# Kernel optimization log

Measured on AMD Instinct MI355X. Metric: run time of the kernel, lower is better.

Reference implementation:

```python
import jax, jax.numpy as jnp
import numpy as np

B, N, K = 4, 2048, 32
CQ, CK, CV = 128, 128, 256
CQ1, CK1 = max(CQ, 32), max(CK, 32)
NUM_GROUPS = 32
EPS = 1e-5


def conv1x1(x, W, b):
    # x: [B,Cin,N,K], W: [Cout,Cin], b: [Cout]
    return jnp.einsum('oc,bcnk->bonk', W, x) + b[None, :, None, None]


def group_norm(x, gamma, beta, num_groups=NUM_GROUPS, eps=EPS):
    # x: [B,C,N,K]; stats over (C//G, N, K) per group, per sample (torch GroupNorm)
    b, c, n, k = x.shape
    xg = x.reshape(b, num_groups, c // num_groups, n, k)
    mean = xg.mean(axis=(2, 3, 4), keepdims=True)
    var = xg.var(axis=(2, 3, 4), keepdims=True)
    xg = (xg - mean) * jax.lax.rsqrt(var + eps)
    x = xg.reshape(b, c, n, k)
    return x * gamma[None, :, None, None] + beta[None, :, None, None]


def setup_inputs() -> dict:
    key = jax.random.key(0)
    ks = jax.random.split(key, 24)
    nrm = lambda k, shape, s=0.05: jax.random.normal(k, shape, jnp.float32) * s
    return {
        'feat': jax.random.normal(ks[0], (B, CQ, N), jnp.float32),
        'grouped_feat': jax.random.normal(ks[1], (B, CK, N, K), jnp.float32),
        'grouped_feat_out': jax.random.normal(ks[2], (B, CV, N, K), jnp.float32),
        'count': jax.random.randint(ks[3], (B, N), 0, K + 1, jnp.int32),
        'W_fc': nrm(ks[4], (CQ1, CQ)), 'b_fc': nrm(ks[5], (CQ1,)),
        'W_gc': nrm(ks[6], (CK1, CK)), 'b_gc': nrm(ks[7], (CK1,)),
        'g1': jnp.ones((CQ1 + CK1,), jnp.float32), 'be1': jnp.zeros((CQ1 + CK1,), jnp.float32),
        'W_w1': nrm(ks[8], (CV, CQ1 + CK1)), 'b_w1': nrm(ks[9], (CV,)),
        'g2': jnp.ones((CV,), jnp.float32), 'be2': jnp.zeros((CV,), jnp.float32),
        'W_w2': nrm(ks[10], (CV, CV)), 'b_w2': nrm(ks[11], (CV,)),
        'W_fo': nrm(ks[12], (CV, CV)), 'b_fo': nrm(ks[13], (CV,)),
        'g3': jnp.ones((CV,), jnp.float32), 'be3': jnp.zeros((CV,), jnp.float32),
    }


def reference(feat, grouped_feat, grouped_feat_out, count,
              W_fc, b_fc, W_gc, b_gc, g1, be1, W_w1, b_w1,
              g2, be2, W_w2, b_w2, W_fo, b_fo, g3, be3):
    # feat_conv (1x1 on [B,CQ,N,1]) then expand along K
    feat1 = jnp.einsum('oc,bcn->bon', W_fc, feat) + b_fc[None, :, None]  # [B,CQ1,N]
    feat1 = jnp.broadcast_to(feat1[..., None], (B, CQ1, N, K))
    gfeat1 = conv1x1(grouped_feat, W_gc, b_gc)  # [B,CK1,N,K]
    total = jnp.concatenate([feat1, gfeat1], axis=1)  # [B,CQ1+CK1,N,K]

    # weight_conv: ReLU -> GN -> Conv -> ReLU -> GN -> Conv
    x = jax.nn.relu(total)
    x = group_norm(x, g1, be1)
    x = conv1x1(x, W_w1, b_w1)
    x = jax.nn.relu(x)
    x = group_norm(x, g2, be2)
    scores = conv1x1(x, W_w2, b_w2)  # [B,CV,N,K]

    # count-based neighbor mask
    cnt = jnp.clip(count, 1, None)
    mask = (jnp.arange(K, dtype=cnt.dtype) < cnt[..., None]).astype(scores.dtype)  # [B,N,K]
    mask = mask[:, None]  # [B,1,N,K]
    scores = scores * mask + (-1e9) * (1.0 - mask)
    weight = jax.nn.softmax(scores, axis=-1)

    # feat_out_conv: Conv -> GN -> ReLU
    gout = conv1x1(grouped_feat_out, W_fo, b_fo)
    gout = jax.nn.relu(group_norm(gout, g3, be3))

    return (gout * weight).sum(axis=-1)  # [B,CV,N]
```

## Files before the change

kernel.cpp:

```cpp
#include <hip/hip_runtime.h>
#include <stdint.h>

#define DEVI __device__ __forceinline__

typedef __attribute__((ext_vector_type(4))) int    i32x4;
typedef __attribute__((ext_vector_type(4))) float  f32x4;
typedef __attribute__((ext_vector_type(8))) __bf16 bf16x8;

static constexpr int BB = 4, NN = 2048, KK = 32, PP = NN * KK;
static constexpr float GEPS = 1e-5f;

DEVI unsigned short f2bf(float f) {
  unsigned u = __builtin_bit_cast(unsigned, f);
  return (unsigned short)((u + 0x7FFFu + ((u >> 16) & 1u)) >> 16);
}
DEVI float bf2f(unsigned short h) {
  unsigned u = (unsigned)h << 16;
  return __builtin_bit_cast(float, u);
}
DEVI uint2 pack4(float a, float b, float c, float d) {
  return make_uint2((unsigned)f2bf(a) | ((unsigned)f2bf(b) << 16),
                    (unsigned)f2bf(c) | ((unsigned)f2bf(d) << 16));
}
DEVI void mfma16(f32x4& d, i32x4 a, i32x4 b) {
  d = __builtin_amdgcn_mfma_f32_16x16x32_bf16(
      __builtin_bit_cast(bf16x8, a), __builtin_bit_cast(bf16x8, b), d, 0, 0, 0);
}

__global__ void prep_kern(const float* Wfc, const float* Wgc, const float* Wfo,
                          unsigned short* dWfc, unsigned short* dWgc, unsigned short* dWfo) {
  int i = blockIdx.x * 256 + threadIdx.x;
  if (i < 16384)       dWfc[i] = f2bf(Wfc[i]);
  else if (i < 32768)  dWgc[i - 16384] = f2bf(Wgc[i - 16384]);
  else if (i < 98304)  dWfo[i - 32768] = f2bf(Wfo[i - 32768]);
}

template<int CIN, int COUT, int MODE, bool RELU>
__global__ __launch_bounds__(256, 2)
void gemm_kern(const void* srcA, const void* srcB,
               const unsigned short* Wmat, const float* bias,
               unsigned short* out, float* stats, int group_base,
               int P, int tiles_per_b, int nblk) {
  constexpr int MW = COUT / 4;
  constexpr int MF = MW / 16;
  constexpr int KS = CIN / 32;
  constexpr int CINP = CIN + 8;
  __shared__ unsigned short tile[64 * CINP];

  const int tid = threadIdx.x;
  const int lane = tid & 63, w = tid >> 6;
  const int l15 = lane & 15, lg = lane >> 4;
  const int b = blockIdx.x / nblk, blk = blockIdx.x % nblk;

  const unsigned short* Wb = (MODE == 1) ? (Wmat + (size_t)b * COUT * CIN) : Wmat;
  const float* biasb = (MODE == 1) ? (bias + b * COUT) : bias;

  i32x4 a[KS][MF];
#pragma unroll
  for (int ks = 0; ks < KS; ++ks)
#pragma unroll
    for (int mf = 0; mf < MF; ++mf)
      a[ks][mf] = *(const i32x4*)(Wb + (size_t)(w * MW + mf * 16 + l15) * CIN + ks * 32 + lg * 8);

  f32x4 bi[MF];
#pragma unroll
  for (int mf = 0; mf < MF; ++mf)
    bi[mf] = *(const f32x4*)(biasb + w * MW + mf * 16 + lg * 4);

  float ssum[MF], ssq[MF];
#pragma unroll
  for (int mf = 0; mf < MF; ++mf) { ssum[mf] = 0.f; ssq[mf] = 0.f; }

  for (int t = blk; t < tiles_per_b; t += nblk) {
    const int p0 = t * 64;
    if (MODE == 0) {
      const float* src = (const float*)srcA + (size_t)b * CIN * P + p0;
      const int cq = tid >> 4, pq = tid & 15;
#pragma unroll
      for (int cblk = 0; cblk < CIN; cblk += 64) {
        f32x4 v[4];
#pragma unroll
        for (int i = 0; i < 4; ++i)
          v[i] = *(const f32x4*)(src + (size_t)(cblk + cq * 4 + i) * (size_t)P + pq * 4);
#pragma unroll
        for (int jj = 0; jj < 4; ++jj) {
          uint2 pk = pack4(v[0][jj], v[1][jj], v[2][jj], v[3][jj]);
          *(uint2*)&tile[(pq * 4 + jj) * CINP + cblk + cq * 4] = pk;
        }
      }
    } else {
      const unsigned short* r1 = (const unsigned short*)srcA;
      const unsigned short* r2 = (const unsigned short*)srcB;
      const int cg = tid & 15, pq = tid >> 4;
#pragma unroll
      for (int cblk = 0; cblk < 256; cblk += 64) {
#pragma unroll
        for (int j = 0; j < 4; ++j) {
          int p = pq * 4 + j;
          const unsigned short* sp;
          if (cblk < 128) {
            int n = (p0 + p) >> 5;
            sp = r1 + ((size_t)b * NN + n) * 128 + cblk + cg * 4;
          } else {
            sp = r2 + ((size_t)b * PP + p0 + p) * 128 + (cblk - 128) + cg * 4;
          }
          *(uint2*)&tile[p * CINP + cblk + cg * 4] = *(const uint2*)sp;
        }
      }
    }
    __syncthreads();

    f32x4 acc[MF][4];
#pragma unroll
    for (int mf = 0; mf < MF; ++mf)
#pragma unroll
      for (int nf = 0; nf < 4; ++nf) acc[mf][nf] = f32x4{0.f, 0.f, 0.f, 0.f};

#pragma unroll
    for (int ks = 0; ks < KS; ++ks) {
      i32x4 bfr[4];
#pragma unroll
      for (int nf = 0; nf < 4; ++nf)
        bfr[nf] = *(const i32x4*)&tile[(nf * 16 + l15) * CINP + ks * 32 + lg * 8];
#pragma unroll
      for (int mf = 0; mf < MF; ++mf)
#pragma unroll
        for (int nf = 0; nf < 4; ++nf) mfma16(acc[mf][nf], a[ks][mf], bfr[nf]);
    }
    __syncthreads();

#pragma unroll
    for (int mf = 0; mf < MF; ++mf) {
      const int o4 = w * MW + mf * 16 + lg * 4;
#pragma unroll
      for (int nf = 0; nf < 4; ++nf) {
        const int p = p0 + nf * 16 + l15;
        float y0 = acc[mf][nf][0] + bi[mf][0];
        float y1 = acc[mf][nf][1] + bi[mf][1];
        float y2 = acc[mf][nf][2] + bi[mf][2];
        float y3 = acc[mf][nf][3] + bi[mf][3];
        if (RELU) {
          y0 = fmaxf(y0, 0.f); y1 = fmaxf(y1, 0.f);
          y2 = fmaxf(y2, 0.f); y3 = fmaxf(y3, 0.f);
        }
        ssum[mf] += y0 + y1 + y2 + y3;
        ssq[mf] += y0 * y0 + y1 * y1 + y2 * y2 + y3 * y3;
        *(uint2*)(out + ((size_t)b * P + p) * COUT + o4) = pack4(y0, y1, y2, y3);
      }
    }
  }

#pragma unroll
  for (int mf = 0; mf < MF; ++mf) {
    float s = ssum[mf], q = ssq[mf];
#pragma unroll
    for (int d = 1; d < 16; d <<= 1) { s += __shfl_xor(s, d); q += __shfl_xor(q, d); }
    if (l15 == 0) {
      int g = group_base + ((w * MW + mf * 16 + lg * 4) >> 3);
      atomicAdd(&stats[(b * 32 + g) * 2 + 0], s);
      atomicAdd(&stats[(b * 32 + g) * 2 + 1], q);
    }
  }
}

__global__ void fold1_kern(const float* st1, const float* g1, const float* be1,
                           const float* W_w1, const float* b_w1,
                           unsigned short* W1p, float* b1p) {
  int b = blockIdx.x, tid = threadIdx.x;
  __shared__ float s_l[256], t_l[256];
  {
    int c = tid, g = c >> 3;
    float cnt = (g < 16) ? (8.f * NN) : (8.f * NN * KK);
    float su = st1[(b * 32 + g) * 2], sq = st1[(b * 32 + g) * 2 + 1];
    float mean = su / cnt;
    float var = fmaxf(sq / cnt - mean * mean, 0.f);
    float s = g1[c] * rsqrtf(var + GEPS);
    s_l[c] = s; t_l[c] = be1[c] - mean * s;
  }
  __syncthreads();
  int o = tid;
  float acc = b_w1[o];
  for (int c = 0; c < 256; ++c) {
    float wv = W_w1[o * 256 + c];
    W1p[((size_t)b * 256 + o) * 256 + c] = f2bf(wv * s_l[c]);
    acc += wv * t_l[c];
  }
  b1p[b * 256 + o] = acc;
}

__global__ void fold23_kern(const float* st2, const float* st3,
                            const float* g2, const float* be2,
                            const float* W_w2, const float* b_w2,
                            const float* g3, const float* be3,
                            unsigned short* W2p, float* b2p, float* s3t3) {
  int b = blockIdx.x, tid = threadIdx.x;
  __shared__ float s_l[256], t_l[256];
  {
    int c = tid, g = c >> 3;
    float cnt = 8.f * NN * KK;
    float su = st2[(b * 32 + g) * 2], sq = st2[(b * 32 + g) * 2 + 1];
    float mean = su / cnt;
    float var = fmaxf(sq / cnt - mean * mean, 0.f);
    float s = g2[c] * rsqrtf(var + GEPS);
    s_l[c] = s; t_l[c] = be2[c] - mean * s;

    float su3 = st3[(b * 32 + g) * 2], sq3 = st3[(b * 32 + g) * 2 + 1];
    float mean3 = su3 / cnt;
    float var3 = fmaxf(sq3 / cnt - mean3 * mean3, 0.f);
    float s3 = g3[c] * rsqrtf(var3 + GEPS);
    s3t3[(b * 256 + c) * 2 + 0] = s3;
    s3t3[(b * 256 + c) * 2 + 1] = be3[c] - mean3 * s3;
  }
  __syncthreads();
  int o = tid;
  float acc = b_w2[o];
  for (int c = 0; c < 256; ++c) {
    float wv = W_w2[o * 256 + c];
    W2p[((size_t)b * 256 + o) * 256 + c] = f2bf(wv * s_l[c]);
    acc += wv * t_l[c];
  }
  b2p[b * 256 + o] = acc;
}

__global__ __launch_bounds__(256, 2)
void k5_kern(const unsigned short* x2t, const unsigned short* gor,
             const unsigned short* W2p, const float* b2p,
             const float* s3t3, const int* count, float* out, int nblk) {
  __shared__ unsigned short xt[64 * 264];
  const int tid = threadIdx.x, lane = tid & 63, w = tid >> 6;
  const int l15 = lane & 15, lg = lane >> 4;
  const int b = blockIdx.x / nblk, blk = blockIdx.x % nblk;

  i32x4 wb[8][4];
  const unsigned short* Wb = W2p + (size_t)b * 65536;
#pragma unroll
  for (int ks = 0; ks < 8; ++ks)
#pragma unroll
    for (int of = 0; of < 4; ++of)
      wb[ks][of] = *(const i32x4*)(Wb + (size_t)(w * 64 + of * 16 + l15) * 256 + ks * 32 + lg * 8);

  float bia[4], s3v[4], t3v[4];
#pragma unroll
  for (int of = 0; of < 4; ++of) {
    int o = w * 64 + of * 16 + l15;
    bia[of] = b2p[b * 256 + o];
    s3v[of] = s3t3[(b * 256 + o) * 2 + 0];
    t3v[of] = s3t3[(b * 256 + o) * 2 + 1];
  }

  const unsigned short* xb = x2t + (size_t)b * PP * 256;
  const unsigned short* gb = gor + (size_t)b * PP * 256;

  for (int t = blk; t < 1024; t += nblk) {
    const int p0 = t * 64, n0 = p0 >> 5;
    {
      const int cg = tid & 15, pq = tid >> 4;
#pragma unroll
      for (int cblk = 0; cblk < 256; cblk += 64)
#pragma unroll
        for (int j = 0; j < 4; ++j) {
          int p = pq * 4 + j;
          *(uint2*)&xt[p * 264 + cblk + cg * 4] =
              *(const uint2*)(xb + (size_t)(p0 + p) * 256 + cblk + cg * 4);
        }
    }
    __syncthreads();

    f32x4 acc[4][4];
#pragma unroll
    for (int pf = 0; pf < 4; ++pf)
#pragma unroll
      for (int of = 0; of < 4; ++of) acc[pf][of] = f32x4{0.f, 0.f, 0.f, 0.f};

#pragma unroll
    for (int ks = 0; ks < 8; ++ks) {
      i32x4 af[4];
#pragma unroll
      for (int pf = 0; pf < 4; ++pf)
        af[pf] = *(const i32x4*)&xt[(pf * 16 + l15) * 264 + ks * 32 + lg * 8];
#pragma unroll
      for (int pf = 0; pf < 4; ++pf)
#pragma unroll
        for (int of = 0; of < 4; ++of) mfma16(acc[pf][of], af[pf], wb[ks][of]);
    }
    __syncthreads();

    const int cnt0 = max(count[b * NN + n0], 1);
    const int cnt1 = max(count[b * NN + n0 + 1], 1);
#pragma unroll
    for (int of = 0; of < 4; ++of) {
      const int o = w * 64 + of * 16 + l15;
      float res[2];
#pragma unroll
      for (int pair = 0; pair < 2; ++pair) {
        const int cnt = pair ? cnt1 : cnt0;
        float sc[2][4];
#pragma unroll
        for (int ph = 0; ph < 2; ++ph)
#pragma unroll
          for (int r = 0; r < 4; ++r) {
            int k = ph * 16 + lg * 4 + r;
            float v = acc[pair * 2 + ph][of][r] + bia[of];
            sc[ph][r] = (k < cnt) ? v : -1e9f;
          }
        float m = sc[0][0];
#pragma unroll
        for (int ph = 0; ph < 2; ++ph)
#pragma unroll
          for (int r = 0; r < 4; ++r) m = fmaxf(m, sc[ph][r]);
        m = fmaxf(m, __shfl_xor(m, 16));
        m = fmaxf(m, __shfl_xor(m, 32));
        float den = 0.f, con = 0.f;
#pragma unroll
        for (int ph = 0; ph < 2; ++ph)
#pragma unroll
          for (int r = 0; r < 4; ++r) {
            float e = __expf(sc[ph][r] - m);
            int p = p0 + pair * 32 + ph * 16 + lg * 4 + r;
            float g = bf2f(gb[(size_t)p * 256 + o]);
            g = fmaxf(s3v[of] * g + t3v[of], 0.f);
            den += e; con += e * g;
          }
        den += __shfl_xor(den, 16); con += __shfl_xor(con, 16);
        den += __shfl_xor(den, 32); con += __shfl_xor(con, 32);
        res[pair] = con / den;
      }
      if (lg == 0)
        *(float2*)(out + (size_t)(b * 256 + o) * NN + n0) = make_float2(res[0], res[1]);
    }
  }
}

extern "C" void kernel_launch(void* const* d_in, const int* in_sizes, int n_in,
                              void* d_out, int out_size, void* d_ws, size_t ws_size,
                              hipStream_t stream) {
  const float* feat = (const float*)d_in[0];
  const float* gf   = (const float*)d_in[1];
  const float* gfo  = (const float*)d_in[2];
  const int*   cnt  = (const int*)d_in[3];
  const float* W_fc = (const float*)d_in[4];
  const float* b_fc = (const float*)d_in[5];
  const float* W_gc = (const float*)d_in[6];
  const float* b_gc = (const float*)d_in[7];
  const float* g1   = (const float*)d_in[8];
  const float* be1  = (const float*)d_in[9];
  const float* W_w1 = (const float*)d_in[10];
  const float* b_w1 = (const float*)d_in[11];
  const float* g2   = (const float*)d_in[12];
  const float* be2  = (const float*)d_in[13];
  const float* W_w2 = (const float*)d_in[14];
  const float* b_w2 = (const float*)d_in[15];
  const float* W_fo = (const float*)d_in[16];
  const float* b_fo = (const float*)d_in[17];
  const float* g3   = (const float*)d_in[18];
  const float* be3  = (const float*)d_in[19];
  float* out = (float*)d_out;
  char* ws = (char*)d_ws;

  constexpr size_t ST1 = 0, ST2 = 1024, ST3 = 2048;
  constexpr size_t WFC = 4096;
  constexpr size_t WGC = WFC + 32768;
  constexpr size_t WFO = WGC + 32768;
  constexpr size_t W1P = WFO + 131072;
  constexpr size_t B1P = W1P + 524288;
  constexpr size_t W2P = B1P + 4096;
  constexpr size_t B2P = W2P + 524288;
  constexpr size_t S3T = B2P + 4096;
  constexpr size_t R1  = 2097152;
  constexpr size_t X2  = R1 + 2097152;
  constexpr size_t R2  = X2 + 134217728;
  constexpr size_t GOR = R2;
  constexpr size_t WS_NEED = GOR + 134217728;
  if (ws_size < WS_NEED) return;

  float* st1 = (float*)(ws + ST1);
  float* st2 = (float*)(ws + ST2);
  float* st3 = (float*)(ws + ST3);
  unsigned short* wfc = (unsigned short*)(ws + WFC);
  unsigned short* wgc = (unsigned short*)(ws + WGC);
  unsigned short* wfo = (unsigned short*)(ws + WFO);
  unsigned short* w1p = (unsigned short*)(ws + W1P);
  float* b1p = (float*)(ws + B1P);
  unsigned short* w2p = (unsigned short*)(ws + W2P);
  float* b2p = (float*)(ws + B2P);
  float* s3t = (float*)(ws + S3T);
  unsigned short* r1 = (unsigned short*)(ws + R1);
  unsigned short* x2 = (unsigned short*)(ws + X2);
  unsigned short* r2 = (unsigned short*)(ws + R2);
  unsigned short* gor = (unsigned short*)(ws + GOR);

  hipMemsetAsync(ws, 0, 3072, stream);
  prep_kern<<<384, 256, 0, stream>>>(W_fc, W_gc, W_fo, wfc, wgc, wfo);

  gemm_kern<128, 128, 0, true><<<dim3(4 * 32), 256, 0, stream>>>(
      feat, nullptr, wfc, b_fc, r1, st1, 0, NN, NN / 64, 32);
  gemm_kern<128, 128, 0, true><<<dim3(4 * 128), 256, 0, stream>>>(
      gf, nullptr, wgc, b_gc, r2, st1, 16, PP, PP / 64, 128);

  fold1_kern<<<4, 256, 0, stream>>>(st1, g1, be1, W_w1, b_w1, w1p, b1p);

  gemm_kern<256, 256, 1, true><<<dim3(4 * 128), 256, 0, stream>>>(
      r1, r2, w1p, b1p, x2, st2, 0, PP, PP / 64, 128);

  gemm_kern<256, 256, 0, false><<<dim3(4 * 128), 256, 0, stream>>>(
      gfo, nullptr, wfo, b_fo, gor, st3, 0, PP, PP / 64, 128);

  fold23_kern<<<4, 256, 0, stream>>>(st2, st3, g2, be2, W_w2, b_w2, g3, be3, w2p, b2p, s3t);

  k5_kern<<<dim3(4 * 128), 256, 0, stream>>>(x2, gor, w2p, b2p, s3t, cnt, out, 128);
}
```

Before: 719.3 us.

## Stream weights per k-step instead of register-caching, raise occupancy and grid sizes

The GEMM and final softmax kernels no longer keep the whole weight matrix resident in registers. They reload weight fragments from global/L2 on every k-step, freeing registers so launch bounds can rise to 3-4 blocks per CU. Grids are widened to match. The MODE 1 GEMM drops LDS staging and reads r1/r2 fragments straight from global. k5 now stages the gout tile in LDS instead of x2, so the softmax epilogue's gather from global becomes an LDS read. The trade-off is more global/L2 traffic for weights and activations in exchange for occupancy and latency hiding.

```diff
diff --git a/kernel.cpp b/kernel.cpp
--- a/kernel.cpp
+++ b/kernel.cpp
@@ -36,7 +36,7 @@
 }
 
 template<int CIN, int COUT, int MODE, bool RELU>
-__global__ __launch_bounds__(256, 2)
+__global__ __launch_bounds__(256, MODE == 1 ? 4 : 3)
 void gemm_kern(const void* srcA, const void* srcB,
                const unsigned short* Wmat, const float* bias,
                unsigned short* out, float* stats, int group_base,
@@ -45,7 +45,7 @@
   constexpr int MF = MW / 16;
   constexpr int KS = CIN / 32;
   constexpr int CINP = CIN + 8;
-  __shared__ unsigned short tile[64 * CINP];
+  __shared__ unsigned short tile[(MODE == 0) ? 64 * CINP : 16];
 
   const int tid = threadIdx.x;
   const int lane = tid & 63, w = tid >> 6;
@@ -54,13 +54,8 @@
 
   const unsigned short* Wb = (MODE == 1) ? (Wmat + (size_t)b * COUT * CIN) : Wmat;
   const float* biasb = (MODE == 1) ? (bias + b * COUT) : bias;
-
-  i32x4 a[KS][MF];
-#pragma unroll
-  for (int ks = 0; ks < KS; ++ks)
-#pragma unroll
-    for (int mf = 0; mf < MF; ++mf)
-      a[ks][mf] = *(const i32x4*)(Wb + (size_t)(w * MW + mf * 16 + l15) * CIN + ks * 32 + lg * 8);
+  const unsigned short* r1b = (const unsigned short*)srcA + (size_t)b * NN * 128;
+  const unsigned short* r2b = (const unsigned short*)srcB + (size_t)b * PP * 128;
 
   f32x4 bi[MF];
 #pragma unroll
@@ -75,59 +70,59 @@
     const int p0 = t * 64;
     if (MODE == 0) {
       const float* src = (const float*)srcA + (size_t)b * CIN * P + p0;
-      const int cq = tid >> 4, pq = tid & 15;
-#pragma unroll
-      for (int cblk = 0; cblk < CIN; cblk += 64) {
-        f32x4 v[4];
-#pragma unroll
-        for (int i = 0; i < 4; ++i)
-          v[i] = *(const f32x4*)(src + (size_t)(cblk + cq * 4 + i) * (size_t)P + pq * 4);
+      const int c16 = tid >> 4, pq = tid & 15;
+#pragma unroll
+      for (int pass = 0; pass < CIN / 128; ++pass) {
+        const int c0 = pass * 128 + c16 * 8;
+        f32x4 v[8];
+#pragma unroll
+        for (int i = 0; i < 8; ++i)
+          v[i] = *(const f32x4*)(src + (size_t)(c0 + i) * (size_t)P + pq * 4);
 #pragma unroll
         for (int jj = 0; jj < 4; ++jj) {
-          uint2 pk = pack4(v[0][jj], v[1][jj], v[2][jj], v[3][jj]);
-          *(uint2*)&tile[(pq * 4 + jj) * CINP + cblk + cq * 4] = pk;
+          uint2 lo = pack4(v[0][jj], v[1][jj], v[2][jj], v[3][jj]);
+          uint2 hi = pack4(v[4][jj], v[5][jj], v[6][jj], v[7][jj]);
+          uint4 q = make_uint4(lo.x, lo.y, hi.x, hi.y);
+          *(uint4*)&tile[(pq * 4 + jj) * CINP + c0] = q;
         }
       }
-    } else {
-      const unsigned short* r1 = (const unsigned short*)srcA;
-      const unsigned short* r2 = (const unsigned short*)srcB;
-      const int cg = tid & 15, pq = tid >> 4;
-#pragma unroll
-      for (int cblk = 0; cblk < 256; cblk += 64) {
-#pragma unroll
-        for (int j = 0; j < 4; ++j) {
-          int p = pq * 4 + j;
-          const unsigned short* sp;
-          if (cblk < 128) {
-            int n = (p0 + p) >> 5;
-            sp = r1 + ((size_t)b * NN + n) * 128 + cblk + cg * 4;
+      __syncthreads();
+    }
+
+    f32x4 acc[MF][4];
+#pragma unroll
+    for (int mf = 0; mf < MF; ++mf)
+#pragma unroll
+      for (int nf = 0; nf < 4; ++nf) acc[mf][nf] = f32x4{0.f, 0.f, 0.f, 0.f};
+
+#pragma unroll
+    for (int ks = 0; ks < KS; ++ks) {
+      i32x4 a4[MF], b4[4];
+#pragma unroll
+      for (int mf = 0; mf < MF; ++mf)
+        a4[mf] = *(const i32x4*)(Wb + (size_t)(w * MW + mf * 16 + l15) * CIN + ks * 32 + lg * 8);
+      if (MODE == 0) {
+#pragma unroll
+        for (int nf = 0; nf < 4; ++nf)
+          b4[nf] = *(const i32x4*)&tile[(nf * 16 + l15) * CINP + ks * 32 + lg * 8];
+      } else {
+#pragma unroll
+        for (int nf = 0; nf < 4; ++nf) {
+          if (ks < 4) {
+            const int n = (p0 >> 5) + (nf >> 1);
+            b4[nf] = *(const i32x4*)(r1b + (size_t)n * 128 + ks * 32 + lg * 8);
           } else {
-            sp = r2 + ((size_t)b * PP + p0 + p) * 128 + (cblk - 128) + cg * 4;
+            b4[nf] = *(const i32x4*)(r2b + (size_t)(p0 + nf * 16 + l15) * 128 +
+                                     (ks - 4) * 32 + lg * 8);
           }
-          *(uint2*)&tile[p * CINP + cblk + cg * 4] = *(const uint2*)sp;
         }
       }
-    }
-    __syncthreads();
-
-    f32x4 acc[MF][4];
-#pragma unroll
-    for (int mf = 0; mf < MF; ++mf)
-#pragma unroll
-      for (int nf = 0; nf < 4; ++nf) acc[mf][nf] = f32x4{0.f, 0.f, 0.f, 0.f};
-
-#pragma unroll
-    for (int ks = 0; ks < KS; ++ks) {
-      i32x4 bfr[4];
-#pragma unroll
-      for (int nf = 0; nf < 4; ++nf)
-        bfr[nf] = *(const i32x4*)&tile[(nf * 16 + l15) * CINP + ks * 32 + lg * 8];
 #pragma unroll
       for (int mf = 0; mf < MF; ++mf)
 #pragma unroll
-        for (int nf = 0; nf < 4; ++nf) mfma16(acc[mf][nf], a[ks][mf], bfr[nf]);
-    }
-    __syncthreads();
+        for (int nf = 0; nf < 4; ++nf) mfma16(acc[mf][nf], a4[mf], b4[nf]);
+    }
+    if (MODE == 0) __syncthreads();
 
 #pragma unroll
     for (int mf = 0; mf < MF; ++mf) {
@@ -222,22 +217,17 @@
   b2p[b * 256 + o] = acc;
 }
 
-__global__ __launch_bounds__(256, 2)
+__global__ __launch_bounds__(256, 3)
 void k5_kern(const unsigned short* x2t, const unsigned short* gor,
              const unsigned short* W2p, const float* b2p,
              const float* s3t3, const int* count, float* out, int nblk) {
-  __shared__ unsigned short xt[64 * 264];
+  constexpr int GP = 272;
+  __shared__ unsigned short gt[64 * GP];
   const int tid = threadIdx.x, lane = tid & 63, w = tid >> 6;
   const int l15 = lane & 15, lg = lane >> 4;
   const int b = blockIdx.x / nblk, blk = blockIdx.x % nblk;
 
-  i32x4 wb[8][4];
   const unsigned short* Wb = W2p + (size_t)b * 65536;
-#pragma unroll
-  for (int ks = 0; ks < 8; ++ks)
-#pragma unroll
-    for (int of = 0; of < 4; ++of)
-      wb[ks][of] = *(const i32x4*)(Wb + (size_t)(w * 64 + of * 16 + l15) * 256 + ks * 32 + lg * 8);
 
   float bia[4], s3v[4], t3v[4];
 #pragma unroll
@@ -253,16 +243,18 @@
 
   for (int t = blk; t < 1024; t += nblk) {
     const int p0 = t * 64, n0 = p0 >> 5;
+
     {
-      const int cg = tid & 15, pq = tid >> 4;
-#pragma unroll
-      for (int cblk = 0; cblk < 256; cblk += 64)
-#pragma unroll
-        for (int j = 0; j < 4; ++j) {
-          int p = pq * 4 + j;
-          *(uint2*)&xt[p * 264 + cblk + cg * 4] =
-              *(const uint2*)(xb + (size_t)(p0 + p) * 256 + cblk + cg * 4);
-        }
+      const unsigned short* gsrc = gb + (size_t)p0 * 256;
+      const int cg = tid & 15, pr4 = (tid >> 4) * 4;
+#pragma unroll
+      for (int j = 0; j < 4; ++j) {
+        const int p = pr4 + j;
+        uint4 q0 = *(const uint4*)(gsrc + (size_t)p * 256 + cg * 8);
+        uint4 q1 = *(const uint4*)(gsrc + (size_t)p * 256 + 128 + cg * 8);
+        *(uint4*)&gt[p * GP + cg * 8] = q0;
+        *(uint4*)&gt[p * GP + 128 + cg * 8] = q1;
+      }
     }
     __syncthreads();
 
@@ -274,16 +266,18 @@
 
 #pragma unroll
     for (int ks = 0; ks < 8; ++ks) {
-      i32x4 af[4];
+      i32x4 af[4], wf[4];
 #pragma unroll
       for (int pf = 0; pf < 4; ++pf)
-        af[pf] = *(const i32x4*)&xt[(pf * 16 + l15) * 264 + ks * 32 + lg * 8];
+        af[pf] = *(const i32x4*)(xb + (size_t)(p0 + pf * 16 + l15) * 256 + ks * 32 + lg * 8);
+#pragma unroll
+      for (int of = 0; of < 4; ++of)
+        wf[of] = *(const i32x4*)(Wb + (size_t)(w * 64 + of * 16 + l15) * 256 + ks * 32 + lg * 8);
 #pragma unroll
       for (int pf = 0; pf < 4; ++pf)
 #pragma unroll
-        for (int of = 0; of < 4; ++of) mfma16(acc[pf][of], af[pf], wb[ks][of]);
-    }
-    __syncthreads();
+        for (int of = 0; of < 4; ++of) mfma16(acc[pf][of], af[pf], wf[of]);
+    }
 
     const int cnt0 = max(count[b * NN + n0], 1);
     const int cnt1 = max(count[b * NN + n0 + 1], 1);
@@ -316,8 +310,8 @@
 #pragma unroll
           for (int r = 0; r < 4; ++r) {
             float e = __expf(sc[ph][r] - m);
-            int p = p0 + pair * 32 + ph * 16 + lg * 4 + r;
-            float g = bf2f(gb[(size_t)p * 256 + o]);
+            int prel = pair * 32 + ph * 16 + lg * 4 + r;
+            float g = bf2f(gt[prel * GP + o]);
             g = fmaxf(s3v[of] * g + t3v[of], 0.f);
             den += e; con += e * g;
           }
@@ -328,6 +322,7 @@
       if (lg == 0)
         *(float2*)(out + (size_t)(b * 256 + o) * NN + n0) = make_float2(res[0], res[1]);
     }
+    __syncthreads();
   }
 }
 
@@ -394,18 +389,18 @@
 
   gemm_kern<128, 128, 0, true><<<dim3(4 * 32), 256, 0, stream>>>(
       feat, nullptr, wfc, b_fc, r1, st1, 0, NN, NN / 64, 32);
-  gemm_kern<128, 128, 0, true><<<dim3(4 * 128), 256, 0, stream>>>(
-      gf, nullptr, wgc, b_gc, r2, st1, 16, PP, PP / 64, 128);
+  gemm_kern<128, 128, 0, true><<<dim3(4 * 192), 256, 0, stream>>>(
+      gf, nullptr, wgc, b_gc, r2, st1, 16, PP, PP / 64, 192);
 
   fold1_kern<<<4, 256, 0, stream>>>(st1, g1, be1, W_w1, b_w1, w1p, b1p);
 
-  gemm_kern<256, 256, 1, true><<<dim3(4 * 128), 256, 0, stream>>>(
-      r1, r2, w1p, b1p, x2, st2, 0, PP, PP / 64, 128);
-
-  gemm_kern<256, 256, 0, false><<<dim3(4 * 128), 256, 0, stream>>>(
-      gfo, nullptr, wfo, b_fo, gor, st3, 0, PP, PP / 64, 128);
+  gemm_kern<256, 256, 1, true><<<dim3(4 * 256), 256, 0, stream>>>(
+      r1, r2, w1p, b1p, x2, st2, 0, PP, PP / 64, 256);
+
+  gemm_kern<256, 256, 0, false><<<dim3(4 * 192), 256, 0, stream>>>(
+      gfo, nullptr, wfo, b_fo, gor, st3, 0, PP, PP / 64, 192);
 
   fold23_kern<<<4, 256, 0, stream>>>(st2, st3, g2, be2, W_w2, b_w2, g3, be3, w2p, b2p, s3t);
 
-  k5_kern<<<dim3(4 * 128), 256, 0, stream>>>(x2, gor, w2p, b2p, s3t, cnt, out, 128);
-}
+  k5_kern<<<dim3(4 * 192), 256, 0, stream>>>(x2, gor, w2p, b2p, s3t, cnt, out, 192);
+}
```

Measured after the change: 1.084 ms. 50.7% more time.

## Double threads per block, split output channels across 8 waves, restage LDS

Applied to the files above, without the earlier changes.

All GEMM kernels and the final softmax kernel move from 256 to 512 threads per block. Each wave now owns half as many output channels, which cuts register-resident weight fragments and is meant to raise occupancy. The final kernel now reads the x2 MFMA operand straight from global memory and stages the gout tile in LDS for the weighted sum, replacing strided bf16 global gathers. Tile loads use 16-byte vector copies, and the fold kernels read weights as float4. The cost is that each weight fragment is reloaded by twice as many waves, the x2 operand reads are uncached, and the changed barrier placement adds risk.

```diff
diff --git a/kernel.cpp b/kernel.cpp
--- a/kernel.cpp
+++ b/kernel.cpp
@@ -36,12 +36,12 @@
 }
 
 template<int CIN, int COUT, int MODE, bool RELU>
-__global__ __launch_bounds__(256, 2)
+__global__ __launch_bounds__(512, 4)
 void gemm_kern(const void* srcA, const void* srcB,
                const unsigned short* Wmat, const float* bias,
                unsigned short* out, float* stats, int group_base,
                int P, int tiles_per_b, int nblk) {
-  constexpr int MW = COUT / 4;
+  constexpr int MW = COUT / 8;
   constexpr int MF = MW / 16;
   constexpr int KS = CIN / 32;
   constexpr int CINP = CIN + 8;
@@ -77,35 +77,33 @@
       const float* src = (const float*)srcA + (size_t)b * CIN * P + p0;
       const int cq = tid >> 4, pq = tid & 15;
 #pragma unroll
-      for (int cblk = 0; cblk < CIN; cblk += 64) {
+      for (int pass = 0; pass < CIN / 128; ++pass) {
+        const int c0 = pass * 128 + cq * 4;
         f32x4 v[4];
 #pragma unroll
         for (int i = 0; i < 4; ++i)
-          v[i] = *(const f32x4*)(src + (size_t)(cblk + cq * 4 + i) * (size_t)P + pq * 4);
-#pragma unroll
-        for (int jj = 0; jj < 4; ++jj) {
-          uint2 pk = pack4(v[0][jj], v[1][jj], v[2][jj], v[3][jj]);
-          *(uint2*)&tile[(pq * 4 + jj) * CINP + cblk + cq * 4] = pk;
-        }
+          v[i] = *(const f32x4*)(src + (size_t)(c0 + i) * (size_t)P + pq * 4);
+#pragma unroll
+        for (int jj = 0; jj < 4; ++jj)
+          *(uint2*)&tile[(pq * 4 + jj) * CINP + c0] =
+              pack4(v[0][jj], v[1][jj], v[2][jj], v[3][jj]);
       }
     } else {
-      const unsigned short* r1 = (const unsigned short*)srcA;
-      const unsigned short* r2 = (const unsigned short*)srcB;
-      const int cg = tid & 15, pq = tid >> 4;
-#pragma unroll
-      for (int cblk = 0; cblk < 256; cblk += 64) {
-#pragma unroll
-        for (int j = 0; j < 4; ++j) {
-          int p = pq * 4 + j;
-          const unsigned short* sp;
-          if (cblk < 128) {
-            int n = (p0 + p) >> 5;
-            sp = r1 + ((size_t)b * NN + n) * 128 + cblk + cg * 4;
-          } else {
-            sp = r2 + ((size_t)b * PP + p0 + p) * 128 + (cblk - 128) + cg * 4;
-          }
-          *(uint2*)&tile[p * CINP + cblk + cg * 4] = *(const uint2*)sp;
+      const unsigned short* r1b = (const unsigned short*)srcA + (size_t)b * NN * 128;
+      const unsigned short* r2b = (const unsigned short*)srcB + (size_t)b * PP * 128;
+      const int p = tid >> 3;
+#pragma unroll
+      for (int j = 0; j < 4; ++j) {
+        const int chunk = j * 8 + (tid & 7);
+        const int c = chunk * 8;
+        const unsigned short* sp;
+        if (c < 128) {
+          const int n = (p0 + p) >> 5;
+          sp = r1b + (size_t)n * 128 + c;
+        } else {
+          sp = r2b + (size_t)(p0 + p) * 128 + (c - 128);
         }
+        *(uint4*)&tile[p * CINP + c] = *(const uint4*)sp;
       }
     }
     __syncthreads();
@@ -118,14 +116,14 @@
 
 #pragma unroll
     for (int ks = 0; ks < KS; ++ks) {
-      i32x4 bfr[4];
+      i32x4 b4[4];
 #pragma unroll
       for (int nf = 0; nf < 4; ++nf)
-        bfr[nf] = *(const i32x4*)&tile[(nf * 16 + l15) * CINP + ks * 32 + lg * 8];
+        b4[nf] = *(const i32x4*)&tile[(nf * 16 + l15) * CINP + ks * 32 + lg * 8];
 #pragma unroll
       for (int mf = 0; mf < MF; ++mf)
 #pragma unroll
-        for (int nf = 0; nf < 4; ++nf) mfma16(acc[mf][nf], a[ks][mf], bfr[nf]);
+        for (int nf = 0; nf < 4; ++nf) mfma16(acc[mf][nf], a[ks][mf], b4[nf]);
     }
     __syncthreads();
 
@@ -180,10 +178,13 @@
   __syncthreads();
   int o = tid;
   float acc = b_w1[o];
-  for (int c = 0; c < 256; ++c) {
-    float wv = W_w1[o * 256 + c];
-    W1p[((size_t)b * 256 + o) * 256 + c] = f2bf(wv * s_l[c]);
-    acc += wv * t_l[c];
+  for (int c4 = 0; c4 < 64; ++c4) {
+    float4 wv = *(const float4*)(W_w1 + o * 256 + c4 * 4);
+    *(uint2*)&W1p[((size_t)b * 256 + o) * 256 + c4 * 4] =
+        pack4(wv.x * s_l[c4 * 4], wv.y * s_l[c4 * 4 + 1],
+              wv.z * s_l[c4 * 4 + 2], wv.w * s_l[c4 * 4 + 3]);
+    acc += wv.x * t_l[c4 * 4] + wv.y * t_l[c4 * 4 + 1] +
+           wv.z * t_l[c4 * 4 + 2] + wv.w * t_l[c4 * 4 + 3];
   }
   b1p[b * 256 + o] = acc;
 }
@@ -214,35 +215,40 @@
   __syncthreads();
   int o = tid;
   float acc = b_w2[o];
-  for (int c = 0; c < 256; ++c) {
-    float wv = W_w2[o * 256 + c];
-    W2p[((size_t)b * 256 + o) * 256 + c] = f2bf(wv * s_l[c]);
-    acc += wv * t_l[c];
+  for (int c4 = 0; c4 < 64; ++c4) {
+    float4 wv = *(const float4*)(W_w2 + o * 256 + c4 * 4);
+    *(uint2*)&W2p[((size_t)b * 256 + o) * 256 + c4 * 4] =
+        pack4(wv.x * s_l[c4 * 4], wv.y * s_l[c4 * 4 + 1],
+              wv.z * s_l[c4 * 4 + 2], wv.w * s_l[c4 * 4 + 3]);
+    acc += wv.x * t_l[c4 * 4] + wv.y * t_l[c4 * 4 + 1] +
+           wv.z * t_l[c4 * 4 + 2] + wv.w * t_l[c4 * 4 + 3];
   }
   b2p[b * 256 + o] = acc;
 }
 
-__global__ __launch_bounds__(256, 2)
+__global__ __launch_bounds__(512, 4)
 void k5_kern(const unsigned short* x2t, const unsigned short* gor,
              const unsigned short* W2p, const float* b2p,
              const float* s3t3, const int* count, float* out, int nblk) {
-  __shared__ unsigned short xt[64 * 264];
+  constexpr int GP = 264;
+  __shared__ unsigned short gt[64 * GP];
   const int tid = threadIdx.x, lane = tid & 63, w = tid >> 6;
   const int l15 = lane & 15, lg = lane >> 4;
   const int b = blockIdx.x / nblk, blk = blockIdx.x % nblk;
 
-  i32x4 wb[8][4];
   const unsigned short* Wb = W2p + (size_t)b * 65536;
+
+  i32x4 wb[8][2];
 #pragma unroll
   for (int ks = 0; ks < 8; ++ks)
 #pragma unroll
-    for (int of = 0; of < 4; ++of)
-      wb[ks][of] = *(const i32x4*)(Wb + (size_t)(w * 64 + of * 16 + l15) * 256 + ks * 32 + lg * 8);
-
-  float bia[4], s3v[4], t3v[4];
-#pragma unroll
-  for (int of = 0; of < 4; ++of) {
-    int o = w * 64 + of * 16 + l15;
+    for (int of = 0; of < 2; ++of)
+      wb[ks][of] = *(const i32x4*)(Wb + (size_t)(w * 32 + of * 16 + l15) * 256 + ks * 32 + lg * 8);
+
+  float bia[2], s3v[2], t3v[2];
+#pragma unroll
+  for (int of = 0; of < 2; ++of) {
+    int o = w * 32 + of * 16 + l15;
     bia[of] = b2p[b * 256 + o];
     s3v[of] = s3t3[(b * 256 + o) * 2 + 0];
     t3v[of] = s3t3[(b * 256 + o) * 2 + 1];
@@ -253,43 +259,41 @@
 
   for (int t = blk; t < 1024; t += nblk) {
     const int p0 = t * 64, n0 = p0 >> 5;
+
     {
-      const int cg = tid & 15, pq = tid >> 4;
-#pragma unroll
-      for (int cblk = 0; cblk < 256; cblk += 64)
-#pragma unroll
-        for (int j = 0; j < 4; ++j) {
-          int p = pq * 4 + j;
-          *(uint2*)&xt[p * 264 + cblk + cg * 4] =
-              *(const uint2*)(xb + (size_t)(p0 + p) * 256 + cblk + cg * 4);
-        }
+      const unsigned short* gsrc = gb + (size_t)p0 * 256;
+      const int p = tid >> 3;
+#pragma unroll
+      for (int j = 0; j < 4; ++j) {
+        const int c = (j * 8 + (tid & 7)) * 8;
+        *(uint4*)&gt[p * GP + c] = *(const uint4*)(gsrc + (size_t)p * 256 + c);
+      }
     }
     __syncthreads();
 
-    f32x4 acc[4][4];
+    f32x4 acc[4][2];
 #pragma unroll
     for (int pf = 0; pf < 4; ++pf)
 #pragma unroll
-      for (int of = 0; of < 4; ++of) acc[pf][of] = f32x4{0.f, 0.f, 0.f, 0.f};
+      for (int of = 0; of < 2; ++of) acc[pf][of] = f32x4{0.f, 0.f, 0.f, 0.f};
 
 #pragma unroll
     for (int ks = 0; ks < 8; ++ks) {
       i32x4 af[4];
 #pragma unroll
       for (int pf = 0; pf < 4; ++pf)
-        af[pf] = *(const i32x4*)&xt[(pf * 16 + l15) * 264 + ks * 32 + lg * 8];
+        af[pf] = *(const i32x4*)(xb + (size_t)(p0 + pf * 16 + l15) * 256 + ks * 32 + lg * 8);
 #pragma unroll
       for (int pf = 0; pf < 4; ++pf)
 #pragma unroll
-        for (int of = 0; of < 4; ++of) mfma16(acc[pf][of], af[pf], wb[ks][of]);
-    }
-    __syncthreads();
+        for (int of = 0; of < 2; ++of) mfma16(acc[pf][of], af[pf], wb[ks][of]);
+    }
 
     const int cnt0 = max(count[b * NN + n0], 1);
     const int cnt1 = max(count[b * NN + n0 + 1], 1);
 #pragma unroll
-    for (int of = 0; of < 4; ++of) {
-      const int o = w * 64 + of * 16 + l15;
+    for (int of = 0; of < 2; ++of) {
+      const int o = w * 32 + of * 16 + l15;
       float res[2];
 #pragma unroll
       for (int pair = 0; pair < 2; ++pair) {
@@ -316,8 +320,8 @@
 #pragma unroll
           for (int r = 0; r < 4; ++r) {
             float e = __expf(sc[ph][r] - m);
-            int p = p0 + pair * 32 + ph * 16 + lg * 4 + r;
-            float g = bf2f(gb[(size_t)p * 256 + o]);
+            int prel = pair * 32 + ph * 16 + lg * 4 + r;
+            float g = bf2f(gt[prel * GP + o]);
             g = fmaxf(s3v[of] * g + t3v[of], 0.f);
             den += e; con += e * g;
           }
@@ -328,6 +332,7 @@
       if (lg == 0)
         *(float2*)(out + (size_t)(b * 256 + o) * NN + n0) = make_float2(res[0], res[1]);
     }
+    __syncthreads();
   }
 }
 
@@ -392,20 +397,20 @@
   hipMemsetAsync(ws, 0, 3072, stream);
   prep_kern<<<384, 256, 0, stream>>>(W_fc, W_gc, W_fo, wfc, wgc, wfo);
 
-  gemm_kern<128, 128, 0, true><<<dim3(4 * 32), 256, 0, stream>>>(
+  gemm_kern<128, 128, 0, true><<<dim3(4 * 32), 512, 0, stream>>>(
       feat, nullptr, wfc, b_fc, r1, st1, 0, NN, NN / 64, 32);
-  gemm_kern<128, 128, 0, true><<<dim3(4 * 128), 256, 0, stream>>>(
+  gemm_kern<128, 128, 0, true><<<dim3(4 * 128), 512, 0, stream>>>(
       gf, nullptr, wgc, b_gc, r2, st1, 16, PP, PP / 64, 128);
 
   fold1_kern<<<4, 256, 0, stream>>>(st1, g1, be1, W_w1, b_w1, w1p, b1p);
 
-  gemm_kern<256, 256, 1, true><<<dim3(4 * 128), 256, 0, stream>>>(
+  gemm_kern<256, 256, 1, true><<<dim3(4 * 128), 512, 0, stream>>>(
       r1, r2, w1p, b1p, x2, st2, 0, PP, PP / 64, 128);
 
-  gemm_kern<256, 256, 0, false><<<dim3(4 * 128), 256, 0, stream>>>(
+  gemm_kern<256, 256, 0, false><<<dim3(4 * 128), 512, 0, stream>>>(
       gfo, nullptr, wfo, b_fo, gor, st3, 0, PP, PP / 64, 128);
 
   fold23_kern<<<4, 256, 0, stream>>>(st2, st3, g2, be2, W_w2, b_w2, g3, be3, w2p, b2p, s3t);
 
-  k5_kern<<<dim3(4 * 128), 256, 0, stream>>>(x2, gor, w2p, b2p, s3t, cnt, out, 128);
-}
+  k5_kern<<<dim3(4 * 128), 512, 0, stream>>>(x2, gor, w2p, b2p, s3t, cnt, out, 128);
+}
```

Result: slower. 775.0 us (+7.7%).
